# Kernel optimization log

Measured on AMD Instinct MI355X. Metric: run time of the kernel, lower is better.

Reference implementation:

```python
import jax, jax.numpy as jnp
import numpy as np

TEMPERATURE = 0.07
EPS = 1e-8  # torch CosineSimilarity eps


def setup_inputs() -> dict:
    key = jax.random.key(0)
    k1, k2, k3 = jax.random.split(key, 3)
    N, D = 8192, 512
    features = jax.random.normal(k1, (N, D), dtype=jnp.float32)
    positive_mask = jax.random.randint(k2, (N, N), 0, 2, dtype=jnp.int32)
    negative_mask = jax.random.randint(k3, (N, N), 0, 2, dtype=jnp.int32)
    return {"features": features, "positive_mask": positive_mask, "negative_mask": negative_mask}


def reference(features, positive_mask, negative_mask):
    N = positive_mask.shape[0]
    self_contrast = 1.0 - jnp.eye(N, dtype=features.dtype)  # zero diagonal
    pos = positive_mask.astype(features.dtype) * self_contrast  # [N, N]
    neg = negative_mask.astype(features.dtype) * self_contrast  # [N, N]

    # cosine similarity via normalized matmul (same math as broadcasted CosineSimilarity)
    norm = jnp.maximum(jnp.linalg.norm(features, axis=1, keepdims=True), EPS)
    fn = features / norm  # [N, D]
    sim = jnp.matmul(fn, fn.T) / TEMPERATURE  # [N, N]

    logits_max = jax.lax.stop_gradient(jnp.max(sim, axis=1, keepdims=True))
    e = jnp.exp(sim - logits_max)  # [N, N]

    positives = e * pos
    log_neg_sum = jnp.log(jnp.sum(e * neg, axis=1, keepdims=True))  # [N, 1]
    log_prob = positives - log_neg_sum  # [N, N] (faithful to source: exp-masked, not log)

    cardinal = jnp.sum(pos, axis=1)
    cardinal = jnp.where(cardinal == 0, 1.0, cardinal)
    log_prob_sum = jnp.sum(log_prob * pos, axis=1)
    loss = -log_prob_sum / cardinal
    return jnp.mean(loss)
```

## Files before the change

kernel.cpp:

```cpp
#include <hip/hip_runtime.h>
#include <hip/hip_bf16.h>
#include <math.h>

#define NN 8192
#define DD 512
#define INV_T 14.285714285714286f

typedef __attribute__((ext_vector_type(8))) short s16x8;
typedef __attribute__((ext_vector_type(4))) float f32x4;
typedef __attribute__((ext_vector_type(4))) int   i32x4;

__device__ __forceinline__ unsigned short f32_to_bf16(float f) {
  unsigned int u = __float_as_uint(f);
  u += 0x7FFFu + ((u >> 16) & 1u);
  return (unsigned short)(u >> 16);
}

__device__ __forceinline__ void async16(const void* g, void* l) {
  __builtin_amdgcn_global_load_lds((__attribute__((address_space(1))) void*)(void*)g,
                                   (__attribute__((address_space(3))) void*)l,
                                   16, 0, 0);
}

__global__ __launch_bounds__(256) void normalize_kernel(const float* __restrict__ f,
                                                        unsigned short* __restrict__ fnb) {
  const int wave = threadIdx.x >> 6;
  const int lane = threadIdx.x & 63;
  const int row  = blockIdx.x * 4 + wave;
  const float* src = f + (size_t)row * DD + lane * 8;
  float4 v0 = *(const float4*)src;
  float4 v1 = *(const float4*)(src + 4);
  float ss = v0.x*v0.x + v0.y*v0.y + v0.z*v0.z + v0.w*v0.w
           + v1.x*v1.x + v1.y*v1.y + v1.z*v1.z + v1.w*v1.w;
  #pragma unroll
  for (int o = 32; o; o >>= 1) ss += __shfl_xor(ss, o);
  const float r = 1.0f / fmaxf(sqrtf(ss), 1e-8f);
  ushort4 a, b;
  a.x = f32_to_bf16(v0.x * r); a.y = f32_to_bf16(v0.y * r);
  a.z = f32_to_bf16(v0.z * r); a.w = f32_to_bf16(v0.w * r);
  b.x = f32_to_bf16(v1.x * r); b.y = f32_to_bf16(v1.y * r);
  b.z = f32_to_bf16(v1.z * r); b.w = f32_to_bf16(v1.w * r);
  unsigned short* dst = fnb + (size_t)row * DD + lane * 8;
  *(ushort4*)dst = a;
  *(ushort4*)(dst + 4) = b;
}

__global__ __launch_bounds__(256, 3) void fused_kernel(const unsigned short* __restrict__ fnb,
                                                       const int* __restrict__ posm,
                                                       const int* __restrict__ negm,
                                                       float* __restrict__ Spos,
                                                       float* __restrict__ Sneg,
                                                       float* __restrict__ Pcnt) {
  const int bid = blockIdx.x;
  int bi = (int)(64.5 - sqrt(64.5 * 64.5 - 2.0 * (double)bid));
  while (64 * bi - bi * (bi - 1) / 2 > bid) --bi;
  while (64 * (bi + 1) - (bi + 1) * bi / 2 <= bid) ++bi;
  const int bj = bi + (bid - (64 * bi - bi * (bi - 1) / 2));
  const int I = bi * 128;
  const int J = bj * 128;
  const bool offdiag = (bi != bj);

  const int tid  = threadIdx.x;
  const int wave = tid >> 6;
  const int lane = tid & 63;
  const int wm = wave >> 1;
  const int wn = wave & 1;
  const int q   = lane >> 4;
  const int c16 = lane & 15;

  __shared__ alignas(16) unsigned short lA[128 * 32];
  __shared__ alignas(16) unsigned short lB[128 * 32];
  __shared__ float sacc[2][128][3];
  for (int t = tid; t < 2 * 128 * 3; t += 256) ((float*)sacc)[t] = 0.f;

  f32x4 acc[4][4];
  const f32x4 z4 = {0.f, 0.f, 0.f, 0.f};
  #pragma unroll
  for (int mt = 0; mt < 4; ++mt)
    #pragma unroll
    for (int nt = 0; nt < 4; ++nt) acc[mt][nt] = z4;

  for (int kk = 0; kk < DD / 32; ++kk) {
    const int k0 = kk * 32;
    #pragma unroll
    for (int c = 0; c < 2; ++c) {
      const int fidx = tid + c * 256;
      const int L    = fidx >> 2;
      const int p    = fidx & 3;
      const int csrc = (p ^ ((L >> 1) & 3)) & 3;
      async16(fnb + (size_t)(I + L) * DD + k0 + csrc * 8, (char*)lA + fidx * 16);
      const int gB = 4 * (L & 31) + (L >> 5);
      async16(fnb + (size_t)(J + gB) * DD + k0 + csrc * 8, (char*)lB + fidx * 16);
    }
    __syncthreads();

    s16x8 aF[4], bF[4];
    #pragma unroll
    for (int t = 0; t < 4; ++t) {
      const int arow = wm * 64 + t * 16 + c16;
      const int apos = (q ^ ((arow >> 1) & 3)) & 3;
      aF[t] = *(const s16x8*)((const char*)lA + arow * 64 + apos * 16);
      const int Lb = (wn * 16 + c16) | (t << 5);
      const int bpos = (q ^ ((Lb >> 1) & 3)) & 3;
      bF[t] = *(const s16x8*)((const char*)lB + Lb * 64 + bpos * 16);
    }
    #pragma unroll
    for (int mt = 0; mt < 4; ++mt)
      #pragma unroll
      for (int nt = 0; nt < 4; ++nt)
        acc[mt][nt] = __builtin_amdgcn_mfma_f32_16x16x32_bf16(aF[mt], bF[nt], acc[mt][nt], 0, 0, 0);
    __syncthreads();
  }

  #pragma unroll
  for (int mt = 0; mt < 4; ++mt)
    #pragma unroll
    for (int nt = 0; nt < 4; ++nt)
      #pragma unroll
      for (int r = 0; r < 4; ++r)
        acc[mt][nt][r] = __expf(acc[mt][nt][r] * INV_T - INV_T);

  const bool hasdiag = (bi == bj) && (wm == wn);
  const int cb = wn * 64 + 4 * c16;

  #pragma unroll
  for (int mt = 0; mt < 4; ++mt) {
    const int rl = wm * 64 + mt * 16 + q * 4;
    i32x4 pv[4], nv[4];
    #pragma unroll
    for (int r = 0; r < 4; ++r) {
      const size_t off = (size_t)(I + rl + r) * NN + J + cb;
      pv[r] = __builtin_nontemporal_load((const i32x4*)(posm + off));
      nv[r] = __builtin_nontemporal_load((const i32x4*)(negm + off));
    }
    #pragma unroll
    for (int r = 0; r < 4; ++r) {
      float dsp = 0.f, dsn = 0.f, dpc = 0.f;
      #pragma unroll
      for (int nt = 0; nt < 4; ++nt) {
        float pf = (float)pv[r][nt];
        float nf = (float)nv[r][nt];
        if (hasdiag && (rl + r == cb + nt)) { pf = 0.f; nf = 0.f; }
        const float e = acc[mt][nt][r];
        dsp = fmaf(e, pf, dsp);
        dsn = fmaf(e, nf, dsn);
        dpc += pf;
      }
      #pragma unroll
      for (int o = 1; o <= 8; o <<= 1) {
        dsp += __shfl_xor(dsp, o);
        dsn += __shfl_xor(dsn, o);
        dpc += __shfl_xor(dpc, o);
      }
      if (c16 == 0) {
        atomicAdd(&sacc[0][rl + r][0], dsp);
        atomicAdd(&sacc[0][rl + r][1], dsn);
        atomicAdd(&sacc[0][rl + r][2], dpc);
      }
    }
  }

  if (offdiag) {
    #pragma unroll
    for (int nt = 0; nt < 4; ++nt) {
      const int trl = cb + nt;
      i32x4 pv[4], nv[4];
      #pragma unroll
      for (int mt = 0; mt < 4; ++mt) {
        const size_t off = (size_t)(J + trl) * NN + I + wm * 64 + mt * 16 + q * 4;
        pv[mt] = __builtin_nontemporal_load((const i32x4*)(posm + off));
        nv[mt] = __builtin_nontemporal_load((const i32x4*)(negm + off));
      }
      float ts = 0.f, tn = 0.f, tp = 0.f;
      #pragma unroll
      for (int mt = 0; mt < 4; ++mt) {
        #pragma unroll
        for (int r = 0; r < 4; ++r) {
          const float e = acc[mt][nt][r];
          ts = fmaf(e, (float)pv[mt][r], ts);
          tn = fmaf(e, (float)nv[mt][r], tn);
          tp += (float)pv[mt][r];
        }
      }
      ts += __shfl_xor(ts, 16); ts += __shfl_xor(ts, 32);
      tn += __shfl_xor(tn, 16); tn += __shfl_xor(tn, 32);
      tp += __shfl_xor(tp, 16); tp += __shfl_xor(tp, 32);
      if (q == 0) {
        atomicAdd(&sacc[1][trl][0], ts);
        atomicAdd(&sacc[1][trl][1], tn);
        atomicAdd(&sacc[1][trl][2], tp);
      }
    }
  }

  __syncthreads();

  const int r = tid & 127;
  if (tid < 128) {
    atomicAdd(&Spos[I + r], sacc[0][r][0]);
    atomicAdd(&Sneg[I + r], sacc[0][r][1]);
    atomicAdd(&Pcnt[I + r], sacc[0][r][2]);
  } else if (offdiag) {
    atomicAdd(&Spos[J + r], sacc[1][r][0]);
    atomicAdd(&Sneg[J + r], sacc[1][r][1]);
    atomicAdd(&Pcnt[J + r], sacc[1][r][2]);
  }
}

__global__ __launch_bounds__(256) void finalize_kernel(const float* __restrict__ Spos,
                                                       const float* __restrict__ Sneg,
                                                       const float* __restrict__ Pcnt,
                                                       float* __restrict__ out) {
  float local = 0.f;
  for (int i = threadIdx.x; i < NN; i += 256) {
    const float sp = Spos[i], sn = Sneg[i], pc = Pcnt[i];
    const float card = (pc == 0.f) ? 1.f : pc;
    local += (logf(sn) * pc - sp) / card;
  }
  #pragma unroll
  for (int o = 32; o; o >>= 1) local += __shfl_xor(local, o);
  __shared__ float red[4];
  if ((threadIdx.x & 63) == 0) red[threadIdx.x >> 6] = local;
  __syncthreads();
  if (threadIdx.x == 0)
    out[0] = (red[0] + red[1] + red[2] + red[3]) * (1.0f / (float)NN);
}

extern "C" void kernel_launch(void* const* d_in, const int* in_sizes, int n_in,
                              void* d_out, int out_size, void* d_ws, size_t ws_size,
                              hipStream_t stream) {
  const float* feat = (const float*)d_in[0];
  const int* posm   = (const int*)d_in[1];
  const int* negm   = (const int*)d_in[2];
  float* out = (float*)d_out;

  char* ws = (char*)d_ws;
  unsigned short* fnb = (unsigned short*)ws;
  float* Spos = (float*)(ws + (size_t)8 * 1024 * 1024);
  float* Sneg = Spos + NN;
  float* Pcnt = Sneg + NN;

  hipMemsetAsync(Spos, 0, 3 * NN * sizeof(float), stream);
  normalize_kernel<<<NN / 4, 256, 0, stream>>>(feat, fnb);
  fused_kernel<<<2080, 256, 0, stream>>>(fnb, posm, negm, Spos, Sneg, Pcnt);
  finalize_kernel<<<1, 256, 0, stream>>>(Spos, Sneg, Pcnt, out);
}
```

Baseline: 548.2 us.

## Pre-pack bf16 features into MFMA fragment layout and load directly from global

The normalize kernel now writes two copies of the normalized bf16 features in layouts that match the MFMA A and B fragment order. The GEMM loop then reads fragments straight from global memory into registers with double buffering, dropping the LDS staging and both barriers per k-step. The memset is folded into the normalize kernel and block ids are remapped across 8 groups, likely for XCD locality. The cost is an extra feature copy, no LDS sharing across waves (more L2 traffic), and higher register pressure. The kernel is probably dominated by streaming the 512MB of masks, so the gain may be small.

```diff
diff --git a/kernel.cpp b/kernel.cpp
--- a/kernel.cpp
+++ b/kernel.cpp
@@ -16,14 +16,12 @@
   return (unsigned short)(u >> 16);
 }
 
-__device__ __forceinline__ void async16(const void* g, void* l) {
-  __builtin_amdgcn_global_load_lds((__attribute__((address_space(1))) void*)(void*)g,
-                                   (__attribute__((address_space(3))) void*)l,
-                                   16, 0, 0);
-}
-
 __global__ __launch_bounds__(256) void normalize_kernel(const float* __restrict__ f,
-                                                        unsigned short* __restrict__ fnb) {
+                                                        unsigned short* __restrict__ PA,
+                                                        unsigned short* __restrict__ PB,
+                                                        float* __restrict__ acc) {
+  if (blockIdx.x < 96) acc[blockIdx.x * 256 + threadIdx.x] = 0.f;
+
   const int wave = threadIdx.x >> 6;
   const int lane = threadIdx.x & 63;
   const int row  = blockIdx.x * 4 + wave;
@@ -40,18 +38,26 @@
   a.z = f32_to_bf16(v0.z * r); a.w = f32_to_bf16(v0.w * r);
   b.x = f32_to_bf16(v1.x * r); b.y = f32_to_bf16(v1.y * r);
   b.z = f32_to_bf16(v1.z * r); b.w = f32_to_bf16(v1.w * r);
-  unsigned short* dst = fnb + (size_t)row * DD + lane * 8;
-  *(ushort4*)dst = a;
-  *(ushort4*)(dst + 4) = b;
-}
-
-__global__ __launch_bounds__(256, 3) void fused_kernel(const unsigned short* __restrict__ fnb,
+
+  const int kk = lane >> 2;
+  const int q  = lane & 3;
+  const size_t ca = ((size_t)((row >> 4) * 16 + kk)) * 64 + (row & 15) * 4 + q;
+  const int g  = (row >> 7) * 8 + ((row >> 6) & 1) * 4 + (row & 3);
+  const size_t cbk = ((size_t)(g * 16 + kk)) * 64 + ((row >> 2) & 15) * 4 + q;
+  ushort4* pa = (ushort4*)(PA + ca * 8);
+  ushort4* pb = (ushort4*)(PB + cbk * 8);
+  pa[0] = a; pa[1] = b;
+  pb[0] = a; pb[1] = b;
+}
+
+__global__ __launch_bounds__(256, 3) void fused_kernel(const unsigned short* __restrict__ PA,
+                                                       const unsigned short* __restrict__ PB,
                                                        const int* __restrict__ posm,
                                                        const int* __restrict__ negm,
                                                        float* __restrict__ Spos,
                                                        float* __restrict__ Sneg,
                                                        float* __restrict__ Pcnt) {
-  const int bid = blockIdx.x;
+  const int bid = (blockIdx.x & 7) * 260 + (blockIdx.x >> 3);
   int bi = (int)(64.5 - sqrt(64.5 * 64.5 - 2.0 * (double)bid));
   while (64 * bi - bi * (bi - 1) / 2 > bid) --bi;
   while (64 * (bi + 1) - (bi + 1) * bi / 2 <= bid) ++bi;
@@ -68,10 +74,15 @@
   const int q   = lane >> 4;
   const int c16 = lane & 15;
 
-  __shared__ alignas(16) unsigned short lA[128 * 32];
-  __shared__ alignas(16) unsigned short lB[128 * 32];
   __shared__ float sacc[2][128][3];
   for (int t = tid; t < 2 * 128 * 3; t += 256) ((float*)sacc)[t] = 0.f;
+  __syncthreads();
+
+  const int lc = c16 * 4 + q;
+  const unsigned short* pa0 = PA + (((size_t)((I >> 4) + wm * 4) * 16) * 64 + lc) * 8;
+  const unsigned short* pb0 = PB + (((size_t)((J >> 7) * 8 + wn * 4) * 16) * 64 + lc) * 8;
+  #define AP(t, kk) ((const s16x8*)(pa0 + ((size_t)(t) * 16 * 64 + (size_t)(kk) * 64) * 8))
+  #define BP(t, kk) ((const s16x8*)(pb0 + ((size_t)(t) * 16 * 64 + (size_t)(kk) * 64) * 8))
 
   f32x4 acc[4][4];
   const f32x4 z4 = {0.f, 0.f, 0.f, 0.f};
@@ -80,37 +91,30 @@
     #pragma unroll
     for (int nt = 0; nt < 4; ++nt) acc[mt][nt] = z4;
 
-  for (int kk = 0; kk < DD / 32; ++kk) {
-    const int k0 = kk * 32;
-    #pragma unroll
-    for (int c = 0; c < 2; ++c) {
-      const int fidx = tid + c * 256;
-      const int L    = fidx >> 2;
-      const int p    = fidx & 3;
-      const int csrc = (p ^ ((L >> 1) & 3)) & 3;
-      async16(fnb + (size_t)(I + L) * DD + k0 + csrc * 8, (char*)lA + fidx * 16);
-      const int gB = 4 * (L & 31) + (L >> 5);
-      async16(fnb + (size_t)(J + gB) * DD + k0 + csrc * 8, (char*)lB + fidx * 16);
-    }
-    __syncthreads();
-
-    s16x8 aF[4], bF[4];
-    #pragma unroll
-    for (int t = 0; t < 4; ++t) {
-      const int arow = wm * 64 + t * 16 + c16;
-      const int apos = (q ^ ((arow >> 1) & 3)) & 3;
-      aF[t] = *(const s16x8*)((const char*)lA + arow * 64 + apos * 16);
-      const int Lb = (wn * 16 + c16) | (t << 5);
-      const int bpos = (q ^ ((Lb >> 1) & 3)) & 3;
-      bF[t] = *(const s16x8*)((const char*)lB + Lb * 64 + bpos * 16);
-    }
+  s16x8 a0[4], b0[4], a1[4], b1[4];
+  #pragma unroll
+  for (int t = 0; t < 4; ++t) { a0[t] = *AP(t, 0); b0[t] = *BP(t, 0); }
+
+  for (int kk = 0; kk < 16; kk += 2) {
+    #pragma unroll
+    for (int t = 0; t < 4; ++t) { a1[t] = *AP(t, kk + 1); b1[t] = *BP(t, kk + 1); }
     #pragma unroll
     for (int mt = 0; mt < 4; ++mt)
       #pragma unroll
       for (int nt = 0; nt < 4; ++nt)
-        acc[mt][nt] = __builtin_amdgcn_mfma_f32_16x16x32_bf16(aF[mt], bF[nt], acc[mt][nt], 0, 0, 0);
-    __syncthreads();
-  }
+        acc[mt][nt] = __builtin_amdgcn_mfma_f32_16x16x32_bf16(a0[mt], b0[nt], acc[mt][nt], 0, 0, 0);
+    if (kk + 2 < 16) {
+      #pragma unroll
+      for (int t = 0; t < 4; ++t) { a0[t] = *AP(t, kk + 2); b0[t] = *BP(t, kk + 2); }
+    }
+    #pragma unroll
+    for (int mt = 0; mt < 4; ++mt)
+      #pragma unroll
+      for (int nt = 0; nt < 4; ++nt)
+        acc[mt][nt] = __builtin_amdgcn_mfma_f32_16x16x32_bf16(a1[mt], b1[nt], acc[mt][nt], 0, 0, 0);
+  }
+  #undef AP
+  #undef BP
 
   #pragma unroll
   for (int mt = 0; mt < 4; ++mt)
@@ -235,13 +239,13 @@
   float* out = (float*)d_out;
 
   char* ws = (char*)d_ws;
-  unsigned short* fnb = (unsigned short*)ws;
-  float* Spos = (float*)(ws + (size_t)8 * 1024 * 1024);
+  unsigned short* PA = (unsigned short*)ws;
+  unsigned short* PB = (unsigned short*)(ws + (size_t)8 * 1024 * 1024);
+  float* Spos = (float*)(ws + (size_t)16 * 1024 * 1024);
   float* Sneg = Spos + NN;
   float* Pcnt = Sneg + NN;
 
-  hipMemsetAsync(Spos, 0, 3 * NN * sizeof(float), stream);
-  normalize_kernel<<<NN / 4, 256, 0, stream>>>(feat, fnb);
-  fused_kernel<<<2080, 256, 0, stream>>>(fnb, posm, negm, Spos, Sneg, Pcnt);
+  normalize_kernel<<<NN / 4, 256, 0, stream>>>(feat, PA, PB, Spos);
+  fused_kernel<<<2080, 256, 0, stream>>>(PA, PB, posm, negm, Spos, Sneg, Pcnt);
   finalize_kernel<<<1, 256, 0, stream>>>(Spos, Sneg, Pcnt, out);
 }
```

Measured after the change: 569.5 us. 1.04x slower.
